# Performance work log

Hardware: AMD Instinct MI355X
Metric: run time of the kernel (lower is better)

The kernel has to match this reference:

```python
import jax, jax.numpy as jnp
import numpy as np

B, S, IK, IV = 16, 2048, 3, 1
D = IK + IV          # input_size = 4
H = 256              # hidden_size
F = 512              # dim_feedforward
L = 2                # num_layers
EPS = 1e-5


def setup_inputs() -> dict:
    key = jax.random.key(0)
    ks = jax.random.split(key, 16)
    n = jax.random.normal
    inp = {
        'KEY': n(ks[0], (B, S, IK), jnp.float32),
        'VALUE': n(ks[1], (B, S, IV), jnp.float32),
        # per-layer kernel-attention projections (stacked on layer axis)
        'Wq': n(ks[2], (L, D, H), jnp.float32) * 0.1,
        'bq': jnp.zeros((L, H), jnp.float32),
        'Wk': n(ks[3], (L, D, H), jnp.float32) * 0.1,
        'bk': jnp.zeros((L, H), jnp.float32),
        'Wv': n(ks[4], (L, D, H), jnp.float32) * 0.1,
        'bv': jnp.zeros((L, H), jnp.float32),
        'Wo': n(ks[5], (L, H, D), jnp.float32) * 0.1,
        'bo': jnp.zeros((L, D), jnp.float32),
        'bw': jnp.ones((L,), jnp.float32),          # Gaussian kernel bandwidth
        # LayerNorm 1
        'g1': jnp.ones((L, D), jnp.float32),
        'be1': jnp.zeros((L, D), jnp.float32),
        # FFN
        'W1': n(ks[6], (L, D, F), jnp.float32) * 0.1,
        'b1': jnp.zeros((L, F), jnp.float32),
        'W2': n(ks[7], (L, F, D), jnp.float32) * 0.1,
        'b2': jnp.zeros((L, D), jnp.float32),
        # LayerNorm 2
        'g2': jnp.ones((L, D), jnp.float32),
        'be2': jnp.zeros((L, D), jnp.float32),
        # final fc: input_size -> input_v
        'Wfc': n(ks[8], (D, IV), jnp.float32) * 0.1,
        'bfc': jnp.zeros((IV,), jnp.float32),
    }
    return inp


def _layernorm(x, g, b):
    m = x.mean(-1, keepdims=True)
    v = ((x - m) ** 2).mean(-1, keepdims=True)
    return (x - m) * jax.lax.rsqrt(v + EPS) * g + b


def reference(KEY, VALUE, Wq, bq, Wk, bk, Wv, bv, Wo, bo, bw,
              g1, be1, W1, b1, W2, b2, g2, be2, Wfc, bfc):
    # positioning: concat coords and values -> [B, S, D]
    X = jnp.concatenate([KEY, VALUE], axis=-1)
    n_layers = Wq.shape[0]
    for i in range(n_layers):
        # Nadaraya-Watson Gaussian kernel attention (madsnn, type='nwd', kernel='gauss')
        Q = X @ Wq[i] + bq[i]                      # [B,S,H]
        K = X @ Wk[i] + bk[i]                      # [B,S,H]
        V = X @ Wv[i] + bv[i]                      # [B,S,H]
        # pairwise squared distances ||q-k||^2, [B,S,S]
        d2 = ((Q * Q).sum(-1)[:, :, None]
              + (K * K).sum(-1)[:, None, :]
              - 2.0 * jnp.einsum('bqh,bkh->bqk', Q, K))
        attn = jax.nn.softmax(-0.5 * d2 * (bw[i] ** 2), axis=-1)
        attn_out = jnp.einsum('bqk,bkh->bqh', attn, V) @ Wo[i] + bo[i]  # [B,S,D]
        # residual + LayerNorm + FFN + residual + LayerNorm (dropout = identity in eval)
        res = _layernorm(X + attn_out, g1[i], be1[i])
        ff = jax.nn.relu(res @ W1[i] + b1[i]) @ W2[i] + b2[i]
        X = _layernorm(res + ff, g2[i], be2[i])
    return X @ Wfc + bfc                            # [B,S,IV]
```

## Files before the change

### kernel.cpp

```cpp
#include <hip/hip_runtime.h>

#define BB 16
#define SS 2048
#define NTOK (BB*SS)
#define FF 512
#define EPSF 1e-5f

#if __has_builtin(__builtin_amdgcn_exp2f)
#define EXP2F(x) __builtin_amdgcn_exp2f(x)
#else
#define EXP2F(x) exp2f(x)
#endif

typedef float v2f __attribute__((ext_vector_type(2)));


__device__ __forceinline__ float wred64(float v) {
#pragma unroll
  for (int m = 32; m > 0; m >>= 1) v += __shfl_xor(v, m, 64);
  return v;
}


__global__ __launch_bounds__(256) void prep_kernel(
    const float* __restrict__ KEY, const float* __restrict__ VALUE,
    const float* __restrict__ Wq, const float* __restrict__ bq,
    const float* __restrict__ Wk, const float* __restrict__ bk,
    const float* __restrict__ Wv, const float* __restrict__ bv,
    const float* __restrict__ Wo, const float* __restrict__ bw,
    const float* __restrict__ W1, const float* __restrict__ b1,
    const float* __restrict__ W2,
    float* __restrict__ sm, float* __restrict__ w1t, float* __restrict__ X0)
{
  const int bid = blockIdx.x;
  if (bid < 128) {
    const int gq = bid*256 + threadIdx.x;
    *(float4*)(X0 + (size_t)gq*4) =
        make_float4(KEY[gq*3 + 0], KEY[gq*3 + 1], KEY[gq*3 + 2], VALUE[gq]);
    return;
  }
  const int i = bid - 128;
  if (threadIdx.x >= 64) return;
  const int lane = threadIdx.x;
  float m4[4][4] = {{0}}, gkk[4][4] = {{0}}, wvo[4][4] = {{0}};
  float akk[4] = {0}, bvo[4] = {0};
  float ck1 = 0.f, ck2 = 0.f;

  for (int h = lane; h < 256; h += 64) {
    float vq[4], vk[4], vv[4], wo4[4];
#pragma unroll
    for (int a = 0; a < 4; ++a) {
      vq[a]  = Wq[(i*4 + a)*256 + h];
      vk[a]  = Wk[(i*4 + a)*256 + h];
      vv[a]  = Wv[(i*4 + a)*256 + h];
      wo4[a] = Wo[(i*256 + h)*4 + a];
    }
    const float bqh = bq[i*256 + h], bkh = bk[i*256 + h], bvh = bv[i*256 + h];
#pragma unroll
    for (int a = 0; a < 4; ++a) {
#pragma unroll
      for (int c = 0; c < 4; ++c) {
        m4[a][c]  = fmaf(vq[a], vk[c], m4[a][c]);
        gkk[a][c] = fmaf(vk[a], vk[c], gkk[a][c]);
        wvo[a][c] = fmaf(vv[a], wo4[c], wvo[a][c]);
      }
      akk[a] = fmaf(vk[a], bqh - bkh, akk[a]);
      bvo[a] = fmaf(bvh, wo4[a], bvo[a]);
    }
    ck1 = fmaf(bqh, bkh, ck1);
    ck2 = fmaf(bkh, bkh, ck2);
  }
#pragma unroll
  for (int a = 0; a < 4; ++a) {
#pragma unroll
    for (int c = 0; c < 4; ++c) {
      m4[a][c]  = wred64(m4[a][c]);
      gkk[a][c] = wred64(gkk[a][c]);
      wvo[a][c] = wred64(wvo[a][c]);
    }
    akk[a] = wred64(akk[a]);
    bvo[a] = wred64(bvo[a]);
  }
  ck1 = wred64(ck1); ck2 = wred64(ck2);

  if (lane == 0) {
    const float bwv = bw[i];
    const float bw2 = bwv * bwv * 1.44269504088896f;
    float* s = sm + i*64;
#pragma unroll
    for (int a = 0; a < 4; ++a) {
#pragma unroll
      for (int c = 0; c < 4; ++c) {
        s[a*4+c]      = bw2 * m4[a][c];
        s[16 + a*4+c] = -0.5f * bw2 * gkk[a][c];
        s[32 + a*4+c] = wvo[a][c];
      }
      s[48+a] = bw2 * akk[a];
      s[52+a] = bvo[a];
    }
    s[56] = bw2 * (ck1 - 0.5f * ck2);
  }
  for (int f = lane; f < FF; f += 64) {
    float* rec = w1t + (i*FF + f)*12;
#pragma unroll
    for (int c = 0; c < 4; ++c) rec[c]   = W1[(i*4 + c)*FF + f];
#pragma unroll
    for (int c = 0; c < 4; ++c) rec[4+c] = W2[(i*FF + f)*4 + c];
    rec[8] = b1[i*FF + f];
    rec[9] = 0.f; rec[10] = 0.f; rec[11] = 0.f;
  }
}

__device__ __forceinline__ void compute_feat(const float x[4], const float* __restrict__ s,
                                             float* __restrict__ featrec)
{
  float P[4], VT[4], tk[4];
#pragma unroll
  for (int a = 0; a < 4; ++a) {
    P[a]  = fmaf(s[a*4+3], x[3], fmaf(s[a*4+2], x[2], fmaf(s[a*4+1], x[1], s[a*4+0]*x[0])));
    tk[a] = fmaf(s[16+a*4+3], x[3], fmaf(s[16+a*4+2], x[2], fmaf(s[16+a*4+1], x[1], s[16+a*4+0]*x[0])));
    VT[a] = s[52+a] + fmaf(s[32+3*4+a], x[3], fmaf(s[32+2*4+a], x[2], fmaf(s[32+1*4+a], x[1], s[32+0*4+a]*x[0])));
  }
  float R = s[56];
#pragma unroll
  for (int a = 0; a < 4; ++a) R = fmaf(tk[a] + s[48+a], x[a], R);
  float4* fp = (float4*)featrec;
  fp[0] = make_float4(P[0], P[1], P[2], P[3]);
  fp[1] = make_float4(VT[0], VT[1], VT[2], VT[3]);
  fp[2] = make_float4(R, 0.f, 0.f, 0.f);
}

__global__ __launch_bounds__(256) void feat_kernel(
    const float* __restrict__ X, const float* __restrict__ sm,
    float* __restrict__ fP, float* __restrict__ fV, float* __restrict__ fR)
{
  const int gq = blockIdx.x*256 + threadIdx.x;
  const float4 xv = *(const float4*)(X + (size_t)gq*4);
  float xr[4] = {xv.x, xv.y, xv.z, xv.w};
  float fr[12];
  compute_feat(xr, sm, fr);
  *(float4*)(fP + (size_t)gq*4) = ((float4*)fr)[0];
  *(float4*)(fV + (size_t)gq*4) = ((float4*)fr)[1];
  fR[gq] = fr[8];
}

__device__ __forceinline__ void ln4(const float t[4], const float* __restrict__ g,
                                    const float* __restrict__ b, float r[4])
{
  const float m = 0.25f*(t[0]+t[1]+t[2]+t[3]);
  const float d0 = t[0]-m, d1 = t[1]-m, d2 = t[2]-m, d3 = t[3]-m;
  const float v = 0.25f*(d0*d0 + d1*d1 + d2*d2 + d3*d3);
  const float sc = rsqrtf(v + EPSF);
  r[0] = fmaf(d0*sc, g[0], b[0]);
  r[1] = fmaf(d1*sc, g[1], b[1]);
  r[2] = fmaf(d2*sc, g[2], b[2]);
  r[3] = fmaf(d3*sc, g[3], b[3]);
}

__global__ __launch_bounds__(512, 4) void layer_kernel(
    const float* __restrict__ X,
    const float* __restrict__ fP, const float* __restrict__ fV, const float* __restrict__ fR,
    const float* __restrict__ w1t, const float* __restrict__ smn,
    const float* __restrict__ bo, const float* __restrict__ g1, const float* __restrict__ be1,
    const float* __restrict__ b2v, const float* __restrict__ g2, const float* __restrict__ be2,
    float* __restrict__ Xout,
    float* __restrict__ foP, float* __restrict__ foV, float* __restrict__ foR,
    const float* __restrict__ Wfc, const float* __restrict__ bfc,
    float* __restrict__ outp, int last)
{
  const int bid = blockIdx.x;
  const int b = bid >> 5, qg = bid & 31;
  const int qbase = (b << 11) + (qg << 6);
  const int kbase0 = (b << 11);
  const int tid = threadIdx.x;
  const int lane = tid & 63, wave = tid >> 6;
  const int j = lane & 31, half = lane >> 5;
  const int slice = wave*2 + half;

  __shared__ float smem[2*512*12];
  float* red  = smem;
  float* ress = smem + 3072;
  float* redf = smem + 3328;

  v2f xq0, xq1, xq2v, xq3;
  {
    const float4 xa = *(const float4*)(X + (size_t)(qbase + 2*j    )*4);
    const float4 xb = *(const float4*)(X + (size_t)(qbase + 2*j + 1)*4);
    xq0  = v2f{xa.x, xb.x}; xq1 = v2f{xa.y, xb.y};
    xq2v = v2f{xa.z, xb.z}; xq3 = v2f{xa.w, xb.w};
  }
  v2f a0xy = v2f{0.f,0.f}, a0zw = v2f{0.f,0.f};
  v2f a1xy = v2f{0.f,0.f}, a1zw = v2f{0.f,0.f};
  v2f ad   = v2f{0.f,0.f};

  float4 sP, sV; float sR;
  {
    const int kk = kbase0 + tid;
    sP = *(const float4*)(fP + (size_t)kk*4);
    sV = *(const float4*)(fV + (size_t)kk*4);
    sR = fR[kk];
  }
  {
    float* d = smem + tid*12;
    *(float4*)d = sP; *(float4*)(d+4) = sV; d[8] = sR;
  }
  __syncthreads();

#pragma unroll
  for (int c = 0; c < 4; ++c) {
    if (c < 3) {
      const int kk = kbase0 + (c+1)*512 + tid;
      sP = *(const float4*)(fP + (size_t)kk*4);
      sV = *(const float4*)(fV + (size_t)kk*4);
      sR = fR[kk];
    }
    const float* kf = smem + (c & 1)*6144 + slice*384;
#pragma unroll 4
    for (int k = 0; k < 32; ++k) {
      const float* rec = kf + k*12;
      const float4 P  = *(const float4*)rec;
      const float4 VT = *(const float4*)(rec + 4);
      const float  R  = rec[8];
      v2f l = __builtin_elementwise_fma(xq0, v2f{P.x, P.x}, v2f{R, R});
      l = __builtin_elementwise_fma(xq1,  v2f{P.y, P.y}, l);
      l = __builtin_elementwise_fma(xq2v, v2f{P.z, P.z}, l);
      l = __builtin_elementwise_fma(xq3,  v2f{P.w, P.w}, l);
      const float e0 = EXP2F(l.x);
      const float e1 = EXP2F(l.y);
      const v2f Vxy = v2f{VT.x, VT.y}, Vzw = v2f{VT.z, VT.w};
      const v2f e0v = v2f{e0, e0}, e1v = v2f{e1, e1};
      a0xy = __builtin_elementwise_fma(e0v, Vxy, a0xy);
      a0zw = __builtin_elementwise_fma(e0v, Vzw, a0zw);
      a1xy = __builtin_elementwise_fma(e1v, Vxy, a1xy);
      a1zw = __builtin_elementwise_fma(e1v, Vzw, a1zw);
      ad += v2f{e0, e1};
    }
    if (c < 3) {
      float* d = smem + ((c+1) & 1)*6144 + tid*12;
      *(float4*)d = sP; *(float4*)(d+4) = sV; d[8] = sR;
    }
    __syncthreads();
  }

  float v10[10] = {a0xy.x, a0xy.y, a0zw.x, a0zw.y,
                   a1xy.x, a1xy.y, a1zw.x, a1zw.y, ad.x, ad.y};
#pragma unroll
  for (int c = 0; c < 10; ++c) v10[c] += __shfl_xor(v10[c], 32, 64);
  if (half == 0) {
    float* rr = red + (wave*32 + j)*12;
    *(float4*)rr       = make_float4(v10[0], v10[1], v10[2], v10[3]);
    *(float4*)(rr + 4) = make_float4(v10[4], v10[5], v10[6], v10[7]);
    rr[8] = v10[8]; rr[9] = v10[9];
  }
  __syncthreads();

  if (tid < 64) {
    const int jj = tid >> 1, p = tid & 1;
    float sv0 = 0.f, sv1 = 0.f, sv2 = 0.f, sv3 = 0.f, sd = 0.f;
#pragma unroll
    for (int w = 0; w < 8; ++w) {
      const float* rr = red + (w*32 + jj)*12;
      const float4 vv = *(const float4*)(rr + p*4);
      sv0 += vv.x; sv1 += vv.y; sv2 += vv.z; sv3 += vv.w;
      sd  += rr[8 + p];
    }
    const float inv = 1.0f / sd;
    const float4 xv = *(const float4*)(X + (size_t)(qbase + tid)*4);
    float t4[4];
    t4[0] = xv.x + fmaf(sv0, inv, bo[0]);
    t4[1] = xv.y + fmaf(sv1, inv, bo[1]);
    t4[2] = xv.z + fmaf(sv2, inv, bo[2]);
    t4[3] = xv.w + fmaf(sv3, inv, bo[3]);
    float r[4];
    ln4(t4, g1, be1, r);
    *(float4*)(ress + tid*4) = make_float4(r[0], r[1], r[2], r[3]);
  }
  __syncthreads();

  const int tok = lane, fc = wave;
  const float4 rv = *(const float4*)(ress + tok*4);
  float fa0 = 0.f, fa1 = 0.f, fa2 = 0.f, fa3 = 0.f;
  const float* wt = w1t + (size_t)fc*64*12;
#pragma unroll 4
  for (int f = 0; f < 64; ++f) {
    const float* rec = wt + f*12;
    const float4 w1r = *(const float4*)rec;
    const float4 w2r = *(const float4*)(rec + 4);
    const float b1f = rec[8];
    float h = fmaf(rv.w, w1r.w, fmaf(rv.z, w1r.z, fmaf(rv.y, w1r.y, fmaf(rv.x, w1r.x, b1f))));
    h = fmaxf(h, 0.f);
    fa0 = fmaf(h, w2r.x, fa0);
    fa1 = fmaf(h, w2r.y, fa1);
    fa2 = fmaf(h, w2r.z, fa2);
    fa3 = fmaf(h, w2r.w, fa3);
  }
  *(float4*)(redf + (fc*64 + tok)*4) = make_float4(fa0, fa1, fa2, fa3);
  __syncthreads();

  if (tid < 64) {
    float t2[4];
#pragma unroll
    for (int c = 0; c < 4; ++c) {
      float s = b2v[c];
#pragma unroll
      for (int k = 0; k < 8; ++k) s += redf[(k*64 + tid)*4 + c];
      t2[c] = ress[tid*4 + c] + s;
    }
    float y[4];
    ln4(t2, g2, be2, y);
    const int gq = qbase + tid;
    if (last) {
      outp[gq] = fmaf(y[3], Wfc[3], fmaf(y[2], Wfc[2], fmaf(y[1], Wfc[1], fmaf(y[0], Wfc[0], bfc[0]))));
    } else {
      *(float4*)(Xout + (size_t)gq*4) = make_float4(y[0], y[1], y[2], y[3]);
      float fr[12];
      compute_feat(y, smn, fr);
      *(float4*)(foP + (size_t)gq*4) = ((float4*)fr)[0];
      *(float4*)(foV + (size_t)gq*4) = ((float4*)fr)[1];
      foR[gq] = fr[8];
    }
  }
}

extern "C" void kernel_launch(void* const* d_in, const int* in_sizes, int n_in,
                              void* d_out, int out_size, void* d_ws, size_t ws_size,
                              hipStream_t stream)
{
  const float* KEY   = (const float*)d_in[0];
  const float* VALUE = (const float*)d_in[1];
  const float* Wq  = (const float*)d_in[2];
  const float* bq  = (const float*)d_in[3];
  const float* Wk  = (const float*)d_in[4];
  const float* bk  = (const float*)d_in[5];
  const float* Wv  = (const float*)d_in[6];
  const float* bv  = (const float*)d_in[7];
  const float* Wo  = (const float*)d_in[8];
  const float* bo  = (const float*)d_in[9];
  const float* bw  = (const float*)d_in[10];
  const float* g1  = (const float*)d_in[11];
  const float* be1 = (const float*)d_in[12];
  const float* W1  = (const float*)d_in[13];
  const float* b1  = (const float*)d_in[14];
  const float* W2  = (const float*)d_in[15];
  const float* b2  = (const float*)d_in[16];
  const float* g2  = (const float*)d_in[17];
  const float* be2 = (const float*)d_in[18];
  const float* Wfc = (const float*)d_in[19];
  const float* bfc = (const float*)d_in[20];
  float* out = (float*)d_out;

  float* w    = (float*)d_ws;
  float* sm   = w;
  float* w1t  = w + 128;
  float* X0   = w + 12416;
  float* X1   = w + 143488;
  float* f0P  = w + 274560;
  float* f0V  = w + 405632;
  float* f0R  = w + 536704;
  float* f1P  = w + 569472;
  float* f1V  = w + 700544;
  float* f1R  = w + 831616;

  prep_kernel<<<130, 256, 0, stream>>>(KEY, VALUE, Wq, bq, Wk, bk, Wv, bv, Wo, bw,
                                       W1, b1, W2, sm, w1t, X0);
  feat_kernel<<<128, 256, 0, stream>>>(X0, sm, f0P, f0V, f0R);

  layer_kernel<<<512, 512, 0, stream>>>(X0, f0P, f0V, f0R, w1t, sm + 64,
      bo, g1, be1, b2, g2, be2,
      X1, f1P, f1V, f1R, Wfc, bfc, out, 0);

  layer_kernel<<<512, 512, 0, stream>>>(X1, f1P, f1V, f1R, w1t + FF*12, sm,
      bo + 4, g1 + 4, be1 + 4, b2 + 4, g2 + 4, be2 + 4,
      X0, f0P, f0V, f0R, Wfc, bfc, out, 1);
}
```

Before: 171.3 us.

## Fuse input packing and first-layer features into layer kernel; use 1024-thread blocks

```diff
diff --git a/kernel.cpp b/kernel.cpp
--- a/kernel.cpp
+++ b/kernel.cpp
@@ -22,25 +22,16 @@
 }
 
 
-__global__ __launch_bounds__(256) void prep_kernel(
-    const float* __restrict__ KEY, const float* __restrict__ VALUE,
+__global__ __launch_bounds__(64) void prep_kernel(
     const float* __restrict__ Wq, const float* __restrict__ bq,
     const float* __restrict__ Wk, const float* __restrict__ bk,
     const float* __restrict__ Wv, const float* __restrict__ bv,
     const float* __restrict__ Wo, const float* __restrict__ bw,
     const float* __restrict__ W1, const float* __restrict__ b1,
     const float* __restrict__ W2,
-    float* __restrict__ sm, float* __restrict__ w1t, float* __restrict__ X0)
+    float* __restrict__ sm, float* __restrict__ w1t)
 {
-  const int bid = blockIdx.x;
-  if (bid < 128) {
-    const int gq = bid*256 + threadIdx.x;
-    *(float4*)(X0 + (size_t)gq*4) =
-        make_float4(KEY[gq*3 + 0], KEY[gq*3 + 1], KEY[gq*3 + 2], VALUE[gq]);
-    return;
-  }
-  const int i = bid - 128;
-  if (threadIdx.x >= 64) return;
+  const int i = blockIdx.x;
   const int lane = threadIdx.x;
   float m4[4][4] = {{0}}, gkk[4][4] = {{0}}, wvo[4][4] = {{0}};
   float akk[4] = {0}, bvo[4] = {0};
@@ -128,20 +119,6 @@
   fp[0] = make_float4(P[0], P[1], P[2], P[3]);
   fp[1] = make_float4(VT[0], VT[1], VT[2], VT[3]);
   fp[2] = make_float4(R, 0.f, 0.f, 0.f);
-}
-
-__global__ __launch_bounds__(256) void feat_kernel(
-    const float* __restrict__ X, const float* __restrict__ sm,
-    float* __restrict__ fP, float* __restrict__ fV, float* __restrict__ fR)
-{
-  const int gq = blockIdx.x*256 + threadIdx.x;
-  const float4 xv = *(const float4*)(X + (size_t)gq*4);
-  float xr[4] = {xv.x, xv.y, xv.z, xv.w};
-  float fr[12];
-  compute_feat(xr, sm, fr);
-  *(float4*)(fP + (size_t)gq*4) = ((float4*)fr)[0];
-  *(float4*)(fV + (size_t)gq*4) = ((float4*)fr)[1];
-  fR[gq] = fr[8];
 }
 
 __device__ __forceinline__ void ln4(const float t[4], const float* __restrict__ g,
@@ -157,16 +134,17 @@
   r[3] = fmaf(d3*sc, g[3], b[3]);
 }
 
-__global__ __launch_bounds__(512, 4) void layer_kernel(
+__global__ __launch_bounds__(1024, 8) void layer_kernel(
+    const float* __restrict__ KEY, const float* __restrict__ VALUE,
     const float* __restrict__ X,
     const float* __restrict__ fP, const float* __restrict__ fV, const float* __restrict__ fR,
-    const float* __restrict__ w1t, const float* __restrict__ smn,
+    const float* __restrict__ w1t, const float* __restrict__ smc, const float* __restrict__ smn,
     const float* __restrict__ bo, const float* __restrict__ g1, const float* __restrict__ be1,
     const float* __restrict__ b2v, const float* __restrict__ g2, const float* __restrict__ be2,
     float* __restrict__ Xout,
     float* __restrict__ foP, float* __restrict__ foV, float* __restrict__ foR,
     const float* __restrict__ Wfc, const float* __restrict__ bfc,
-    float* __restrict__ outp, int last)
+    float* __restrict__ outp, int first, int last)
 {
   const int bid = blockIdx.x;
   const int b = bid >> 5, qg = bid & 31;
@@ -176,14 +154,22 @@
   const int lane = tid & 63, wave = tid >> 6;
   const int j = lane & 31, half = lane >> 5;
   const int slice = wave*2 + half;
+  const int s512 = tid & 511;
+  const bool loP = (tid < 512);
 
   __shared__ float smem[2*512*12];
   float* red  = smem;
-  float* ress = smem + 3072;
-  float* redf = smem + 3328;
+  float* ress = smem + 6144;
+  float* redf = smem + 6400;
 
   v2f xq0, xq1, xq2v, xq3;
-  {
+  if (first) {
+    const int qa = qbase + 2*j, qb = qa + 1;
+    xq0  = v2f{KEY[qa*3    ], KEY[qb*3    ]};
+    xq1  = v2f{KEY[qa*3 + 1], KEY[qb*3 + 1]};
+    xq2v = v2f{KEY[qa*3 + 2], KEY[qb*3 + 2]};
+    xq3  = v2f{VALUE[qa], VALUE[qb]};
+  } else {
     const float4 xa = *(const float4*)(X + (size_t)(qbase + 2*j    )*4);
     const float4 xb = *(const float4*)(X + (size_t)(qbase + 2*j + 1)*4);
     xq0  = v2f{xa.x, xb.x}; xq1 = v2f{xa.y, xb.y};
@@ -194,29 +180,66 @@
   v2f ad   = v2f{0.f,0.f};
 
   float4 sP, sV; float sR;
+  float sx0, sx1, sx2, sx3;
+
   {
-    const int kk = kbase0 + tid;
-    sP = *(const float4*)(fP + (size_t)kk*4);
-    sV = *(const float4*)(fV + (size_t)kk*4);
-    sR = fR[kk];
+    const int kk = kbase0 + s512;
+    if (first) {
+      sx0 = KEY[kk*3]; sx1 = KEY[kk*3+1]; sx2 = KEY[kk*3+2]; sx3 = VALUE[kk];
+    } else if (loP) {
+      sP = *(const float4*)(fP + (size_t)kk*4);
+    } else {
+      sV = *(const float4*)(fV + (size_t)kk*4);
+      sR = fR[kk];
+    }
   }
   {
-    float* d = smem + tid*12;
-    *(float4*)d = sP; *(float4*)(d+4) = sV; d[8] = sR;
+    float* d = smem + s512*12;
+    if (first) {
+      const float x0 = sx0, x1 = sx1, x2 = sx2, x3 = sx3;
+      if (loP) {
+        float P[4];
+#pragma unroll
+        for (int a = 0; a < 4; ++a)
+          P[a] = fmaf(smc[a*4+3], x3, fmaf(smc[a*4+2], x2, fmaf(smc[a*4+1], x1, smc[a*4+0]*x0)));
+        *(float4*)d = make_float4(P[0], P[1], P[2], P[3]);
+      } else {
+        float VT[4], tk[4], xr[4] = {x0, x1, x2, x3};
+        float R = smc[56];
+#pragma unroll
+        for (int a = 0; a < 4; ++a) {
+          tk[a] = fmaf(smc[16+a*4+3], x3, fmaf(smc[16+a*4+2], x2, fmaf(smc[16+a*4+1], x1, smc[16+a*4+0]*x0)));
+          VT[a] = smc[52+a] + fmaf(smc[32+3*4+a], x3, fmaf(smc[32+2*4+a], x2, fmaf(smc[32+1*4+a], x1, smc[32+0*4+a]*x0)));
+        }
+#pragma unroll
+        for (int a = 0; a < 4; ++a) R = fmaf(tk[a] + smc[48+a], xr[a], R);
+        *(float4*)(d+4) = make_float4(VT[0], VT[1], VT[2], VT[3]);
+        d[8] = R;
+      }
+    } else if (loP) {
+      *(float4*)d = sP;
+    } else {
+      *(float4*)(d+4) = sV; d[8] = sR;
+    }
   }
   __syncthreads();
 
 #pragma unroll
   for (int c = 0; c < 4; ++c) {
     if (c < 3) {
-      const int kk = kbase0 + (c+1)*512 + tid;
-      sP = *(const float4*)(fP + (size_t)kk*4);
-      sV = *(const float4*)(fV + (size_t)kk*4);
-      sR = fR[kk];
-    }
-    const float* kf = smem + (c & 1)*6144 + slice*384;
+      const int kk = kbase0 + (c+1)*512 + s512;
+      if (first) {
+        sx0 = KEY[kk*3]; sx1 = KEY[kk*3+1]; sx2 = KEY[kk*3+2]; sx3 = VALUE[kk];
+      } else if (loP) {
+        sP = *(const float4*)(fP + (size_t)kk*4);
+      } else {
+        sV = *(const float4*)(fV + (size_t)kk*4);
+        sR = fR[kk];
+      }
+    }
+    const float* kf = smem + (c & 1)*6144 + slice*192;
 #pragma unroll 4
-    for (int k = 0; k < 32; ++k) {
+    for (int k = 0; k < 16; ++k) {
       const float* rec = kf + k*12;
       const float4 P  = *(const float4*)rec;
       const float4 VT = *(const float4*)(rec + 4);
@@ -236,8 +259,33 @@
       ad += v2f{e0, e1};
     }
     if (c < 3) {
-      float* d = smem + ((c+1) & 1)*6144 + tid*12;
-      *(float4*)d = sP; *(float4*)(d+4) = sV; d[8] = sR;
+      float* d = smem + ((c+1) & 1)*6144 + s512*12;
+      if (first) {
+        const float x0 = sx0, x1 = sx1, x2 = sx2, x3 = sx3;
+        if (loP) {
+          float P[4];
+#pragma unroll
+          for (int a = 0; a < 4; ++a)
+            P[a] = fmaf(smc[a*4+3], x3, fmaf(smc[a*4+2], x2, fmaf(smc[a*4+1], x1, smc[a*4+0]*x0)));
+          *(float4*)d = make_float4(P[0], P[1], P[2], P[3]);
+        } else {
+          float VT[4], tk[4], xr[4] = {x0, x1, x2, x3};
+          float R = smc[56];
+#pragma unroll
+          for (int a = 0; a < 4; ++a) {
+            tk[a] = fmaf(smc[16+a*4+3], x3, fmaf(smc[16+a*4+2], x2, fmaf(smc[16+a*4+1], x1, smc[16+a*4+0]*x0)));
+            VT[a] = smc[52+a] + fmaf(smc[32+3*4+a], x3, fmaf(smc[32+2*4+a], x2, fmaf(smc[32+1*4+a], x1, smc[32+0*4+a]*x0)));
+          }
+#pragma unroll
+          for (int a = 0; a < 4; ++a) R = fmaf(tk[a] + smc[48+a], xr[a], R);
+          *(float4*)(d+4) = make_float4(VT[0], VT[1], VT[2], VT[3]);
+          d[8] = R;
+        }
+      } else if (loP) {
+        *(float4*)d = sP;
+      } else {
+        *(float4*)(d+4) = sV; d[8] = sR;
+      }
     }
     __syncthreads();
   }
@@ -258,19 +306,26 @@
     const int jj = tid >> 1, p = tid & 1;
     float sv0 = 0.f, sv1 = 0.f, sv2 = 0.f, sv3 = 0.f, sd = 0.f;
 #pragma unroll
-    for (int w = 0; w < 8; ++w) {
+    for (int w = 0; w < 16; ++w) {
       const float* rr = red + (w*32 + jj)*12;
       const float4 vv = *(const float4*)(rr + p*4);
       sv0 += vv.x; sv1 += vv.y; sv2 += vv.z; sv3 += vv.w;
       sd  += rr[8 + p];
     }
     const float inv = 1.0f / sd;
-    const float4 xv = *(const float4*)(X + (size_t)(qbase + tid)*4);
+    float xv0, xv1, xv2, xv3;
+    if (first) {
+      const int gq = qbase + tid;
+      xv0 = KEY[gq*3]; xv1 = KEY[gq*3+1]; xv2 = KEY[gq*3+2]; xv3 = VALUE[gq];
+    } else {
+      const float4 xv = *(const float4*)(X + (size_t)(qbase + tid)*4);
+      xv0 = xv.x; xv1 = xv.y; xv2 = xv.z; xv3 = xv.w;
+    }
     float t4[4];
-    t4[0] = xv.x + fmaf(sv0, inv, bo[0]);
-    t4[1] = xv.y + fmaf(sv1, inv, bo[1]);
-    t4[2] = xv.z + fmaf(sv2, inv, bo[2]);
-    t4[3] = xv.w + fmaf(sv3, inv, bo[3]);
+    t4[0] = xv0 + fmaf(sv0, inv, bo[0]);
+    t4[1] = xv1 + fmaf(sv1, inv, bo[1]);
+    t4[2] = xv2 + fmaf(sv2, inv, bo[2]);
+    t4[3] = xv3 + fmaf(sv3, inv, bo[3]);
     float r[4];
     ln4(t4, g1, be1, r);
     *(float4*)(ress + tid*4) = make_float4(r[0], r[1], r[2], r[3]);
@@ -280,9 +335,9 @@
   const int tok = lane, fc = wave;
   const float4 rv = *(const float4*)(ress + tok*4);
   float fa0 = 0.f, fa1 = 0.f, fa2 = 0.f, fa3 = 0.f;
-  const float* wt = w1t + (size_t)fc*64*12;
+  const float* wt = w1t + (size_t)fc*32*12;
 #pragma unroll 4
-  for (int f = 0; f < 64; ++f) {
+  for (int f = 0; f < 32; ++f) {
     const float* rec = wt + f*12;
     const float4 w1r = *(const float4*)rec;
     const float4 w2r = *(const float4*)(rec + 4);
@@ -303,7 +358,7 @@
     for (int c = 0; c < 4; ++c) {
       float s = b2v[c];
 #pragma unroll
-      for (int k = 0; k < 8; ++k) s += redf[(k*64 + tid)*4 + c];
+      for (int k = 0; k < 16; ++k) s += redf[(k*64 + tid)*4 + c];
       t2[c] = ress[tid*4 + c] + s;
     }
     float y[4];
@@ -352,24 +407,21 @@
   float* w    = (float*)d_ws;
   float* sm   = w;
   float* w1t  = w + 128;
-  float* X0   = w + 12416;
-  float* X1   = w + 143488;
-  float* f0P  = w + 274560;
-  float* f0V  = w + 405632;
-  float* f0R  = w + 536704;
-  float* f1P  = w + 569472;
-  float* f1V  = w + 700544;
-  float* f1R  = w + 831616;
-
-  prep_kernel<<<130, 256, 0, stream>>>(KEY, VALUE, Wq, bq, Wk, bk, Wv, bv, Wo, bw,
-                                       W1, b1, W2, sm, w1t, X0);
-  feat_kernel<<<128, 256, 0, stream>>>(X0, sm, f0P, f0V, f0R);
-
-  layer_kernel<<<512, 512, 0, stream>>>(X0, f0P, f0V, f0R, w1t, sm + 64,
+  float* X1   = w + 12416;
+  float* f1P  = w + 143488;
+  float* f1V  = w + 274560;
+  float* f1R  = w + 405632;
+
+  prep_kernel<<<2, 64, 0, stream>>>(Wq, bq, Wk, bk, Wv, bv, Wo, bw,
+                                    W1, b1, W2, sm, w1t);
+
+  layer_kernel<<<512, 1024, 0, stream>>>(KEY, VALUE, X1, f1P, f1V, f1R,
+      w1t, sm, sm + 64,
       bo, g1, be1, b2, g2, be2,
-      X1, f1P, f1V, f1R, Wfc, bfc, out, 0);
-
-  layer_kernel<<<512, 512, 0, stream>>>(X1, f1P, f1V, f1R, w1t + FF*12, sm,
+      X1, f1P, f1V, f1R, Wfc, bfc, out, 1, 0);
+
+  layer_kernel<<<512, 1024, 0, stream>>>(KEY, VALUE, X1, f1P, f1V, f1R,
+      w1t + FF*12, sm + 64, sm,
       bo + 4, g1 + 4, be1 + 4, b2 + 4, g2 + 4, be2 + 4,
-      X0, f0P, f0V, f0R, Wfc, bfc, out, 1);
-}
+      X1, f1P, f1V, f1R, Wfc, bfc, out, 0, 1);
+}
```

Measured after the change: 176.4 us. 1.03x slower.
